# Performance work log

Measured on AMD Instinct MI355X. Metric: run time of the kernel, lower is better.

The kernel has to match this reference:

```python
import jax, jax.numpy as jnp
from jax import lax
import numpy as np

B, M, C, H, W = 32, 2, 256, 16, 16
N = H * W            # 256, square case required by the original bmm chain
DIM = 256            # hardcoded self.dim in the module
THR = 0.1
RATIO = 0.8


def conv2d(x, w, b):
    y = lax.conv_general_dilated(x, w, (1, 1), 'SAME',
                                 dimension_numbers=('NCHW', 'OIHW', 'NCHW'))
    return y + b[None, :, None, None]


def setup_inputs() -> dict:
    key = jax.random.key(0)
    ks = jax.random.split(key, 8)
    return {
        'con_feat': jax.random.normal(ks[0], (B, M, C, H, W), jnp.float32),
        'feat_s':   jax.random.normal(ks[1], (B, M, C, C), jnp.float32),
        'feat_v':   jax.random.uniform(ks[2], (B, M, C), jnp.float32),
        'feat_d':   jax.random.normal(ks[3], (B, M, N, N), jnp.float32),
        'w_enc':    jax.random.normal(ks[4], (C, C, 3, 3), jnp.float32) * 0.02,
        'b_enc':    jnp.zeros((C,), jnp.float32),
        'w_dec':    jax.random.normal(ks[5], (C, C, 3, 3), jnp.float32) * 0.02,
        'b_dec':    jnp.zeros((C,), jnp.float32),
        'w_val':    jax.random.normal(ks[6], (1, 2 * C, 3, 3), jnp.float32) * 0.02,
        'b_val':    jnp.zeros((1,), jnp.float32),
    }


def _assemble(fs, fv, fd, counts):
    # fs: (M,C,C) row blocks, fv: (M,C) diag values, fd: (M,N,N) col blocks, counts: (M,)
    big = max(C, N)                                  # out-of-range sentinel -> dropped
    off = jnp.cumsum(counts) - counts                # exclusive prefix offsets (M,)
    r = jnp.arange(C)
    dest = off[:, None] + r[None, :]                 # (M,C) destination slots
    valid = (r[None, :] < counts[:, None]) & (dest >= 0)
    dest = jnp.where(valid, dest, big).reshape(-1)   # (M*C,)
    ns = jnp.zeros((C, C), fs.dtype).at[dest].set(fs.reshape(M * C, C), mode='drop')
    fd_cols = fd[:, :, :C].transpose(0, 2, 1).reshape(M * C, N)  # source columns as rows
    ndT = jnp.zeros((N, N), fd.dtype).at[dest].set(fd_cols, mode='drop')
    nv = jnp.zeros((C, N), fv.dtype).at[dest, dest].set(fv.reshape(-1), mode='drop')
    return ns, nv, ndT.T


def reference(con_feat, feat_s, feat_v, feat_d, w_enc, b_enc, w_dec, b_dec, w_val, b_val):
    x = con_feat.reshape(B * M, C, H, W)
    # autoencoder reconstruction loss (training branch)
    mid = jax.nn.relu(conv2d(x, w_enc, b_enc))
    x_rec = conv2d(mid, w_dec, b_dec)
    auto_enc_loss = jnp.mean((x - x_rec) ** 2)

    # data-dependent rank budget per (batch, modality)
    counts = jnp.sum(feat_v > THR, axis=-1).astype(jnp.int32)      # (B,M)
    total = jnp.sum(counts, axis=-1)                               # (B,)
    kmin = min(C, N)
    adj = jnp.round(kmin * counts.astype(jnp.float32)
                    / jnp.maximum(total, 1)[:, None].astype(jnp.float32)).astype(jnp.int32)
    if M > 1:
        adj = adj.at[:, -1].set(DIM - jnp.sum(adj[:, :-1], axis=-1))
    counts = jnp.maximum(jnp.where((total > kmin)[:, None], adj, counts), 0)

    # scatter-assemble s/v/d and reconstruct
    ns, nv, nd = jax.vmap(_assemble)(feat_s, feat_v, feat_d, counts)
    rec = jnp.matmul(jnp.matmul(ns, nv), nd)                        # (B,C,N)
    rec = rec.reshape(B, C, H, W)
    rec = conv2d(rec, w_dec, b_dec)                                 # decoder
    rec = (rec - rec.min()) / (rec.max() - rec.min()) * 2.0 - 1.0

    # per-modality value scores, softmax over modality
    scores = jnp.stack([
        jax.nn.sigmoid(jax.nn.relu(conv2d(
            jnp.concatenate([rec, con_feat[:, m]], axis=1), w_val, b_val)))
        for m in range(M)
    ], axis=1)                                                      # (B,M,1,H,W)
    scores = jax.nn.softmax(scores, axis=1)
    fused = jnp.sum((1.0 - RATIO) * scores * con_feat, axis=1) + rec * RATIO
    return fused, auto_enc_loss
```

## Files before the change

kernel.cpp:

```cpp
#include <hip/hip_runtime.h>
#include <math.h>


typedef __attribute__((ext_vector_type(8))) short short8;
typedef __attribute__((ext_vector_type(4))) float f32x4;

__device__ __forceinline__ void gload_lds16(const void* g, void* l) {
  __builtin_amdgcn_global_load_lds(
      (const __attribute__((address_space(1))) void*)g,
      (__attribute__((address_space(3))) void*)l, 16, 0, 0);
}

__device__ __forceinline__ unsigned short f2bf(float f) {
  unsigned u = __float_as_uint(f);
  unsigned r = (u + 0x7FFFu + ((u >> 16) & 1u)) >> 16;
  return (unsigned short)r;
}

__device__ __forceinline__ unsigned mapf(float f) {
  unsigned u = __float_as_uint(f);
  return (u & 0x80000000u) ? ~u : (u | 0x80000000u);
}
__device__ __forceinline__ float unmapf(unsigned u) {
  unsigned v = (u & 0x80000000u) ? (u & 0x7fffffffu) : ~u;
  return __uint_as_float(v);
}

__global__ __launch_bounds__(256) void prep_k(
    const float* __restrict__ cf, const float* __restrict__ we,
    const float* __restrict__ wd, const float* __restrict__ fv,
    unsigned short* __restrict__ Xp, unsigned short* __restrict__ WrE,
    unsigned short* __restrict__ WrD, int* __restrict__ smr,
    float* __restrict__ vd, float4* __restrict__ sraw4,
    float* __restrict__ lacc, unsigned* __restrict__ mm) {
  const int bx = blockIdx.x, t = threadIdx.x;
  if (bx < 2048) {
    int idx = bx * 256 + t;
    int p = idx & 255, ch = (idx >> 8) & 31, img = idx >> 13;
    int ic0 = ch * 8;
    const float* sp = cf + (size_t)img * 65536 + (size_t)ic0 * 256 + p;
    unsigned short h[8];
#pragma unroll
    for (int i = 0; i < 8; ++i) h[i] = f2bf(sp[i * 256]);
    int y = p >> 4, x = p & 15;
    uint4 u;
    u.x = h[0] | (h[1] << 16); u.y = h[2] | (h[3] << 16);
    u.z = h[4] | (h[5] << 16); u.w = h[6] | (h[7] << 16);
    *(uint4*)&Xp[(size_t)img * 82944 + (size_t)(y * 18 + x + 19) * 256 + ic0] = u;
  } else if (bx < 2624) {
    int idx = (bx - 2048) * 256 + t;
    int ch = idx & 31, rest = idx >> 5;
    int s = rest % 9, ocx = rest / 9;
    int oc = ocx & 255, cv = ocx >> 8;
    const float* w = cv ? wd : we;
    unsigned short* o = cv ? WrD : WrE;
    int ic0 = ch * 8;
    unsigned short h[8];
#pragma unroll
    for (int i = 0; i < 8; ++i) h[i] = f2bf(w[(size_t)oc * 2304 + (ic0 + i) * 9 + s]);
    uint4 u;
    u.x = h[0] | (h[1] << 16); u.y = h[2] | (h[3] << 16);
    u.z = h[4] | (h[5] << 16); u.w = h[6] | (h[7] << 16);
    *(uint4*)&o[(size_t)oc * 2304 + s * 256 + ic0] = u;
  } else if (bx < 2752) {
    int img = bx - 2624;
    uint4* base = (uint4*)Xp + (size_t)img * 10368;
    uint4 z; z.x = z.y = z.z = z.w = 0;
    for (int it = t; it < 2176; it += 256) {
      int px = it >> 5, c = it & 31;
      int y, x;
      if (px < 18)      { y = 0;  x = px; }
      else if (px < 36) { y = 17; x = px - 18; }
      else if (px < 52) { y = px - 35; x = 0; }
      else              { y = px - 51; x = 17; }
      base[(y * 18 + x) * 32 + c] = z;
    }
  } else if (bx < 2784) {
    const int b = bx - 2752;
    const float v0 = fv[(size_t)b * 512 + t];
    const float v1 = fv[(size_t)b * 512 + 256 + t];
    const unsigned long long bal0 = __ballot(v0 > 0.1f);
    const unsigned long long bal1 = __ballot(v1 > 0.1f);
    __shared__ int cnt0[4], cnt1[4], fc[2];
    const int wid = t >> 6, lane = t & 63;
    if (lane == 0) { cnt0[wid] = __popcll(bal0); cnt1[wid] = __popcll(bal1); }
    smr[b * 256 + t] = -1;
    vd[b * 256 + t] = 0.f;
    __syncthreads();
    if (t == 0) {
      int c0 = cnt0[0] + cnt0[1] + cnt0[2] + cnt0[3];
      int c1 = cnt1[0] + cnt1[1] + cnt1[2] + cnt1[3];
      int total = c0 + c1;
      int f0, f1;
      if (total > 256) {
        int a0 = (int)rintf(256.0f * (float)c0 / (float)total);
        f0 = a0; f1 = 256 - a0;
      } else { f0 = c0; f1 = c1; }
      fc[0] = max(f0, 0); fc[1] = max(f1, 0);
    }
    __syncthreads();
    const int c0 = fc[0], c1 = fc[1];
    if (t < c0) { smr[b * 256 + t] = t; vd[b * 256 + t] = v0; }
    if (t < c1) {
      int d = c0 + t;
      if (d < 256) { smr[b * 256 + d] = 256 + t; vd[b * 256 + d] = v1; }
    }
  } else {
    int z = bx - 2784;
    if (z < 24) {
      float4 zz; zz.x = zz.y = zz.z = zz.w = 0.f;
      sraw4[z * 256 + t] = zz;
    } else if (t == 0) {
      lacc[0] = 0.f; mm[0] = 0xFFFFFFFFu; mm[1] = 0u;
    }
  }
}

__global__ __launch_bounds__(256) void ansbmt_k(
    const float* __restrict__ fs, const float* __restrict__ fd,
    const int* __restrict__ smr, const float* __restrict__ vd,
    unsigned short* __restrict__ Ans, unsigned short* __restrict__ BmT,
    unsigned short* __restrict__ Recp) {
  const int bx = blockIdx.x, t = threadIdx.x;
  if (bx < 1024) {
    int idx = bx * 256 + t;
    int ch = idx & 31, c = (idx >> 5) & 255, b = idx >> 13;
    int j0 = ch * 8;
    int si = smr[b * 256 + c];
    unsigned short h[8] = {0, 0, 0, 0, 0, 0, 0, 0};
    if (si >= 0) {
      int m = si >> 8, r = si & 255;
      const float* fp = fs + (((size_t)b * 2 + m) * 256 + r) * 256 + j0;
      const float* vp = vd + b * 256 + j0;
#pragma unroll
      for (int i = 0; i < 8; ++i) h[i] = f2bf(fp[i] * vp[i]);
    }
    uint4 u;
    u.x = h[0] | (h[1] << 16); u.y = h[2] | (h[3] << 16);
    u.z = h[4] | (h[5] << 16); u.w = h[6] | (h[7] << 16);
    *(uint4*)&Ans[(size_t)b * 65536 + c * 256 + j0] = u;
  } else if (bx < 1152) {
    __shared__ float sIn[4096];
    const int b = (bx - 1024) >> 2, bz = (bx - 1024) & 3;
    const int sp = smr[b * 256 + t];
    const int m_p = sp >> 8, r_p = sp & 255;
    for (int jg = bz * 8; jg < bz * 8 + 8; ++jg) {
      __syncthreads();
#pragma unroll
      for (int u = 0; u < 4; ++u) {
        int q = t * 4 + u;
        int rr = q >> 6, w = q & 63;
        int m = rr >> 3, i = rr & 7;
        float4 f = ((const float4*)fd)[((size_t)(b * 2 + m) * 256 + jg * 8 + i) * 64 + w];
        *(float4*)&sIn[i * 512 + m * 256 + w * 4] = f;
      }
      __syncthreads();
      unsigned short h[8] = {0, 0, 0, 0, 0, 0, 0, 0};
      if (sp >= 0) {
#pragma unroll
        for (int i = 0; i < 8; ++i) h[i] = f2bf(sIn[i * 512 + m_p * 256 + r_p]);
      }
      uint4 u;
      u.x = h[0] | (h[1] << 16); u.y = h[2] | (h[3] << 16);
      u.z = h[4] | (h[5] << 16); u.w = h[6] | (h[7] << 16);
      *(uint4*)&BmT[(size_t)b * 65536 + t * 256 + jg * 8] = u;
    }
  } else {
    int img = bx - 1152;
    uint4* base = (uint4*)Recp + (size_t)img * 10368;
    uint4 z; z.x = z.y = z.z = z.w = 0;
    for (int it = t; it < 2176; it += 256) {
      int px = it >> 5, c = it & 31;
      int y, x;
      if (px < 18)      { y = 0;  x = px; }
      else if (px < 36) { y = 17; x = px - 18; }
      else if (px < 52) { y = px - 35; x = 0; }
      else              { y = px - 51; x = 17; }
      base[(y * 18 + x) * 32 + c] = z;
    }
  }
}


__global__ __launch_bounds__(512, 4) void encrec_k(
    const unsigned short* __restrict__ Xin, const unsigned short* __restrict__ Wr,
    const float* __restrict__ bias, unsigned short* __restrict__ Midp,
    const unsigned short* __restrict__ BmT, const unsigned short* __restrict__ Ans,
    unsigned short* __restrict__ Recp) {
  __shared__ __align__(16) char S[65536];
  const int t = threadIdx.x, lane = t & 63, wave = t >> 6;
  const int ksplit = wave >> 2, wq = wave & 3;
  const int mw = wq >> 1, nw = wq & 1;
  const int mlane = lane & 15, quad = lane >> 4;
  const int L = blockIdx.x;
  const bool isConv = L < 256;

  int img = 0, b = 0, pt, ot, nkits;
  const char *Ag, *Bg;
  int laneA[2], laneB[2];
  if (isConv) {
    int xcd = L & 7, sl = L >> 3;
    img = xcd * 8 + (sl & 7);
    int tile = sl >> 3;
    pt = tile >> 1; ot = tile & 1;
    Ag = (const char*)Xin + (size_t)img * 165888;
    Bg = (const char*)Wr;
#pragma unroll
    for (int r = 0; r < 2; ++r) {
      int id = r * 512 + t;
      int row = id >> 3, sub = id & 7, q = sub ^ (row & 7);
      int p = pt * 128 + row, y = p >> 4, x = p & 15;
      laneA[r] = (y * 18 + x) * 512 + q * 16;
      laneB[r] = (ot * 128 + row) * 4608 + q * 16;
    }
    nkits = 36;
  } else {
    int l2 = L - 256;
    b = l2 >> 2;
    int tile = l2 & 3;
    pt = tile >> 1; ot = tile & 1;
    Ag = (const char*)BmT + (size_t)b * 131072;
    Bg = (const char*)Ans + (size_t)b * 131072;
#pragma unroll
    for (int r = 0; r < 2; ++r) {
      int id = r * 512 + t;
      int row = id >> 3, sub = id & 7, q = sub ^ (row & 7);
      laneA[r] = (pt * 128 + row) * 512 + q * 16;
      laneB[r] = (ot * 128 + row) * 512 + q * 16;
    }
    nkits = 4;
  }

  int aoff[4], boff[4];
#pragma unroll
  for (int i = 0; i < 4; ++i) {
    int rowm = mw * 64 + i * 16 + mlane;
    aoff[i] = rowm * 128 + (((ksplit * 4 + quad) ^ (rowm & 7)) * 16);
    int rown = nw * 64 + i * 16 + mlane;
    boff[i] = 16384 + rown * 128 + (((ksplit * 4 + quad) ^ (rown & 7)) * 16);
  }

  auto stage = [&](int kit, int buf) {
    int aG, bG = kit * 128;
    if (isConv) {
      int s = kit >> 2;
      int dy = s / 3, dx = s - dy * 3;
      aG = (dy * 18 + dx) * 512 + (kit & 3) * 128;
    } else {
      aG = kit * 128;
    }
    char* dst = S + buf * 32768;
#pragma unroll
    for (int r = 0; r < 2; ++r)
      gload_lds16(Ag + laneA[r] + aG, dst + r * 8192 + wave * 1024);
#pragma unroll
    for (int r = 0; r < 2; ++r)
      gload_lds16(Bg + laneB[r] + bG, dst + 16384 + r * 8192 + wave * 1024);
  };

  f32x4 acc[4][4] = {};
  for (int preload = 0; preload < 1; ++preload) stage(0, 0);
  for (int kit = 0; kit < nkits; ++kit) {
    int cur = kit & 1;
    asm volatile("s_waitcnt vmcnt(0)" ::: "memory");
    asm volatile("s_barrier" ::: "memory");
    if (kit + 1 < nkits) stage(kit + 1, 1 - cur);
    const char* Sb = S + cur * 32768;
    short8 af[4], bf[4];
#pragma unroll
    for (int i = 0; i < 4; ++i) {
      af[i] = *(const short8*)(Sb + aoff[i]);
      bf[i] = *(const short8*)(Sb + boff[i]);
    }
#pragma unroll
    for (int i = 0; i < 4; ++i)
#pragma unroll
      for (int n = 0; n < 4; ++n)
        acc[i][n] = __builtin_amdgcn_mfma_f32_16x16x32_bf16(af[i], bf[n], acc[i][n], 0, 0, 0);
  }

  __syncthreads();
  if (ksplit == 1) {
#pragma unroll
    for (int i = 0; i < 4; ++i)
#pragma unroll
      for (int n = 0; n < 4; ++n)
        *(f32x4*)(S + wq * 16384 + (i * 4 + n) * 1024 + lane * 16) = acc[i][n];
  }
  __syncthreads();
  if (ksplit == 0) {
#pragma unroll
    for (int i = 0; i < 4; ++i)
#pragma unroll
      for (int n = 0; n < 4; ++n)
        acc[i][n] += *(const f32x4*)(S + wq * 16384 + (i * 4 + n) * 1024 + lane * 16);
    if (isConv) {
#pragma unroll
      for (int i = 0; i < 4; ++i) {
        int m0 = pt * 128 + mw * 64 + i * 16 + quad * 4;
#pragma unroll
        for (int n = 0; n < 4; ++n) {
          int oc = ot * 128 + nw * 64 + n * 16 + mlane;
          float bv = bias[oc];
#pragma unroll
          for (int r = 0; r < 4; ++r) {
            int p = m0 + r;
            int y = p >> 4, x = p & 15;
            float v = fmaxf(acc[i][n][r] + bv, 0.f);
            Midp[(size_t)img * 82944 + (size_t)(y * 18 + x + 19) * 256 + oc] = f2bf(v);
          }
        }
      }
    } else {
#pragma unroll
      for (int i = 0; i < 4; ++i) {
        int m0 = pt * 128 + mw * 64 + i * 16 + quad * 4;
#pragma unroll
        for (int n = 0; n < 4; ++n) {
          int cc = ot * 128 + nw * 64 + n * 16 + mlane;
#pragma unroll
          for (int r = 0; r < 4; ++r) {
            int p = m0 + r;
            int y = p >> 4, x = p & 15;
            Recp[(size_t)b * 82944 + (size_t)(y * 18 + x + 19) * 256 + cc] = f2bf(acc[i][n][r]);
          }
        }
      }
    }
  }
}

__global__ __launch_bounds__(512, 4) void conv_dec_k(
    const unsigned short* __restrict__ Midp, const unsigned short* __restrict__ Recp,
    const unsigned short* __restrict__ Wr, const float* __restrict__ bias,
    const float* __restrict__ cfref, float* __restrict__ rec2,
    float* __restrict__ lacc, unsigned* __restrict__ mm) {
  __shared__ __align__(16) char S[65536];
  __shared__ float sred[4], smn[4], smx[4];
  const int t = threadIdx.x, lane = t & 63, wave = t >> 6;
  const int ksplit = wave >> 2, wq = wave & 3;
  const int mw = wq >> 1, nw = wq & 1;
  const int mlane = lane & 15, quad = lane >> 4;
  const int L = blockIdx.x;
  const int xcd = L & 7, sl = L >> 3;
  const int u12 = sl % 12, tile = sl / 12;
  const int unit = xcd * 12 + u12;
  const bool isLoss = unit < 64;
  const int pt = tile >> 1, ot = tile & 1;

  int laneA[2], laneB[2];
#pragma unroll
  for (int r = 0; r < 2; ++r) {
    int id = r * 512 + t;
    int row = id >> 3, sub = id & 7, q = sub ^ (row & 7);
    int p = pt * 128 + row, y = p >> 4, x = p & 15;
    laneA[r] = (y * 18 + x) * 512 + q * 16;
    laneB[r] = (ot * 128 + row) * 4608 + q * 16;
  }
  const char* Ag = isLoss ? (const char*)Midp + (size_t)unit * 165888
                          : (const char*)Recp + (size_t)(unit - 64) * 165888;
  const char* Bg = (const char*)Wr;

  int aoff[4], boff[4];
#pragma unroll
  for (int i = 0; i < 4; ++i) {
    int rowm = mw * 64 + i * 16 + mlane;
    aoff[i] = rowm * 128 + (((ksplit * 4 + quad) ^ (rowm & 7)) * 16);
    int rown = nw * 64 + i * 16 + mlane;
    boff[i] = 16384 + rown * 128 + (((ksplit * 4 + quad) ^ (rown & 7)) * 16);
  }

  auto stage = [&](int kit, int buf) {
    int s = kit >> 2;
    int dy = s / 3, dx = s - dy * 3;
    int aG = (dy * 18 + dx) * 512 + (kit & 3) * 128;
    int bG = kit * 128;
    char* dst = S + buf * 32768;
#pragma unroll
    for (int r = 0; r < 2; ++r)
      gload_lds16(Ag + laneA[r] + aG, dst + r * 8192 + wave * 1024);
#pragma unroll
    for (int r = 0; r < 2; ++r)
      gload_lds16(Bg + laneB[r] + bG, dst + 16384 + r * 8192 + wave * 1024);
  };

  f32x4 acc[4][4] = {};
  stage(0, 0);
  for (int kit = 0; kit < 36; ++kit) {
    int cur = kit & 1;
    asm volatile("s_waitcnt vmcnt(0)" ::: "memory");
    asm volatile("s_barrier" ::: "memory");
    if (kit + 1 < 36) stage(kit + 1, 1 - cur);
    const char* Sb = S + cur * 32768;
    short8 af[4], bf[4];
#pragma unroll
    for (int i = 0; i < 4; ++i) {
      af[i] = *(const short8*)(Sb + aoff[i]);
      bf[i] = *(const short8*)(Sb + boff[i]);
    }
#pragma unroll
    for (int i = 0; i < 4; ++i)
#pragma unroll
      for (int n = 0; n < 4; ++n)
        acc[i][n] = __builtin_amdgcn_mfma_f32_16x16x32_bf16(af[i], bf[n], acc[i][n], 0, 0, 0);
  }

  __syncthreads();
  if (ksplit == 1) {
#pragma unroll
    for (int i = 0; i < 4; ++i)
#pragma unroll
      for (int n = 0; n < 4; ++n)
        *(f32x4*)(S + wq * 16384 + (i * 4 + n) * 1024 + lane * 16) = acc[i][n];
  }
  __syncthreads();
  if (ksplit == 0) {
#pragma unroll
    for (int i = 0; i < 4; ++i)
#pragma unroll
      for (int n = 0; n < 4; ++n)
        acc[i][n] += *(const f32x4*)(S + wq * 16384 + (i * 4 + n) * 1024 + lane * 16);

    if (isLoss) {
      float ls = 0.f;
#pragma unroll
      for (int i = 0; i < 4; ++i) {
        int m0 = pt * 128 + mw * 64 + i * 16 + quad * 4;
#pragma unroll
        for (int n = 0; n < 4; ++n) {
          int oc = ot * 128 + nw * 64 + n * 16 + mlane;
          float bv = bias[oc];
          float4 c4 = *(const float4*)(cfref + (size_t)unit * 65536 + (size_t)oc * 256 + m0);
          float d0 = acc[i][n][0] + bv - c4.x;
          float d1 = acc[i][n][1] + bv - c4.y;
          float d2 = acc[i][n][2] + bv - c4.z;
          float d3 = acc[i][n][3] + bv - c4.w;
          ls += d0 * d0 + d1 * d1 + d2 * d2 + d3 * d3;
        }
      }
#pragma unroll
      for (int off = 32; off; off >>= 1) ls += __shfl_down(ls, off);
      if (lane == 0) sred[wq] = ls;
    } else {
      const int img2 = unit - 64;
      float mn = INFINITY, mx = -INFINITY;
#pragma unroll
      for (int i = 0; i < 4; ++i) {
        int m0 = pt * 128 + mw * 64 + i * 16 + quad * 4;
#pragma unroll
        for (int n = 0; n < 4; ++n) {
          int oc = ot * 128 + nw * 64 + n * 16 + mlane;
          float bv = bias[oc];
          float4 v;
          v.x = acc[i][n][0] + bv; v.y = acc[i][n][1] + bv;
          v.z = acc[i][n][2] + bv; v.w = acc[i][n][3] + bv;
          mn = fminf(mn, fminf(fminf(v.x, v.y), fminf(v.z, v.w)));
          mx = fmaxf(mx, fmaxf(fmaxf(v.x, v.y), fmaxf(v.z, v.w)));
          *(float4*)(rec2 + (size_t)img2 * 65536 + (size_t)oc * 256 + m0) = v;
        }
      }
#pragma unroll
      for (int off = 32; off; off >>= 1) {
        mn = fminf(mn, __shfl_down(mn, off));
        mx = fmaxf(mx, __shfl_down(mx, off));
      }
      if (lane == 0) { smn[wq] = mn; smx[wq] = mx; }
    }
  }
  __syncthreads();
  if (t == 0) {
    if (isLoss) {
      atomicAdd(lacc, sred[0] + sred[1] + sred[2] + sred[3]);
    } else {
      float a = fminf(fminf(smn[0], smn[1]), fminf(smn[2], smn[3]));
      float b2 = fmaxf(fmaxf(smx[0], smx[1]), fmaxf(smx[2], smx[3]));
      atomicMin(&mm[0], mapf(a));
      atomicMax(&mm[1], mapf(b2));
    }
  }
}

__global__ __launch_bounds__(256) void score_conv_k(
    const float* __restrict__ rec2, const float* __restrict__ cf,
    const float* __restrict__ wval, const unsigned* __restrict__ mm,
    float* __restrict__ sraw) {
  const int b = blockIdx.x, phase = blockIdx.y, icc = blockIdx.z;
  const int t = threadIdx.x;
  const int row = t >> 4, col = t & 15;
  __shared__ float s_in[8 * 360];
  __shared__ float s_wv[72];
  for (int i = t; i < 8 * 360; i += 256) s_in[i] = 0.f;
  const float* src;
  float sc = 1.f, sh = 0.f;
  int wofs;
  if (phase == 0) {
    src = rec2 + (size_t)b * 65536;
    float mn = unmapf(mm[0]), mx = unmapf(mm[1]);
    sc = 2.f / (mx - mn);
    sh = -mn * sc - 1.f;
    wofs = 0;
  } else {
    src = cf + ((size_t)b * 2 + (phase - 1)) * 65536;
    wofs = 2304;
  }
  float acc = 0.f;
  for (int ic0 = icc * 32; ic0 < icc * 32 + 32; ic0 += 8) {
    __syncthreads();
#pragma unroll
    for (int i = 0; i < 8; ++i) {
      float v = src[(ic0 + i) * 256 + t];
      if (phase == 0) v = fmaf(v, sc, sh);
      s_in[i * 360 + (row + 1) * 20 + (col + 1)] = v;
    }
    if (t < 72) s_wv[t] = wval[wofs + ic0 * 9 + t];
    __syncthreads();
#pragma unroll
    for (int i = 0; i < 8; ++i)
#pragma unroll
      for (int ky = 0; ky < 3; ++ky)
#pragma unroll
        for (int kx = 0; kx < 3; ++kx)
          acc += s_in[i * 360 + (row + ky) * 20 + (col + kx)] * s_wv[i * 9 + ky * 3 + kx];
  }
  atomicAdd(&sraw[((size_t)b * 3 + phase) * 256 + t], acc);
}

__global__ void fuse_k(const float* __restrict__ cf, const float* __restrict__ rec2,
                       const float* __restrict__ sraw, const float* __restrict__ bval,
                       const unsigned* __restrict__ mm, const float* __restrict__ lacc,
                       float* __restrict__ outp) {
  const int idx = blockIdx.x * 256 + threadIdx.x;
  const int b = idx >> 16;
  const int rest = idx & 65535;
  const int pos = idx & 255;
  const float mn = unmapf(mm[0]), mx = unmapf(mm[1]);
  const float sc = 2.f / (mx - mn), sh = -mn * sc - 1.f;
  const float srec = sraw[(size_t)b * 768 + pos];
  const float sc0 = sraw[(size_t)b * 768 + 256 + pos];
  const float sc1 = sraw[(size_t)b * 768 + 512 + pos];
  const float bv = bval[0];
  const float z0 = fmaxf(srec + sc0 + bv, 0.f);
  const float z1 = fmaxf(srec + sc1 + bv, 0.f);
  const float s0 = 1.f / (1.f + expf(-z0));
  const float s1 = 1.f / (1.f + expf(-z1));
  const float w0 = 1.f / (1.f + expf(s1 - s0));
  const float w1 = 1.f - w0;
  const float rn = fmaf(rec2[idx], sc, sh);
  const float f0 = cf[(size_t)b * 131072 + rest];
  const float f1 = cf[(size_t)b * 131072 + 65536 + rest];
  outp[idx] = 0.2f * (w0 * f0 + w1 * f1) + 0.8f * rn;
  if (idx == 0) outp[2097152] = lacc[0] * (1.f / 4194304.f);
}

extern "C" void kernel_launch(void* const* d_in, const int* in_sizes, int n_in,
                              void* d_out, int out_size, void* d_ws, size_t ws_size,
                              hipStream_t stream) {
  const float* cf    = (const float*)d_in[0];
  const float* fs    = (const float*)d_in[1];
  const float* fv    = (const float*)d_in[2];
  const float* fd    = (const float*)d_in[3];
  const float* w_enc = (const float*)d_in[4];
  const float* b_enc = (const float*)d_in[5];
  const float* w_dec = (const float*)d_in[6];
  const float* b_dec = (const float*)d_in[7];
  const float* w_val = (const float*)d_in[8];
  const float* b_val = (const float*)d_in[9];
  float* out = (float*)d_out;
  float* wsf = (float*)d_ws;

  unsigned short* Xp   = (unsigned short*)wsf;
  unsigned short* Midp = (unsigned short*)(wsf + 2654208);
  unsigned short* Recp = (unsigned short*)(wsf + 5308416);
  float* rec2 = wsf + 6635520;
  unsigned short* WrE = (unsigned short*)(wsf + 8732672);
  unsigned short* WrD = (unsigned short*)(wsf + 9027584);
  unsigned short* Ans = (unsigned short*)(wsf + 9322496);
  unsigned short* BmT = (unsigned short*)(wsf + 10371072);
  float* sraw = wsf + 11419648;
  float* vd   = wsf + 11444224;
  int*   smr  = (int*)(wsf + 11452416);
  float* lacc = wsf + 11460608;
  unsigned* mm = (unsigned*)(wsf + 11460609);

  prep_k<<<2809, 256, 0, stream>>>(cf, w_enc, w_dec, fv, Xp, WrE, WrD, smr, vd,
                                   (float4*)sraw, lacc, mm);
  ansbmt_k<<<1184, 256, 0, stream>>>(fs, fd, smr, vd, Ans, BmT, Recp);
  encrec_k<<<384, 512, 0, stream>>>(Xp, WrE, b_enc, Midp, BmT, Ans, Recp);
  conv_dec_k<<<384, 512, 0, stream>>>(Midp, Recp, WrD, b_dec, cf, rec2, lacc, mm);
  score_conv_k<<<dim3(32, 3, 8), 256, 0, stream>>>(rec2, cf, w_val, mm, sraw);
  fuse_k<<<8192, 256, 0, stream>>>(cf, rec2, sraw, b_val, mm, lacc, out);
}
```

Measured before the change: 217.2 us.

## Fuse prep stages, load GEMM B operand to registers, split score conv

Merges the slot-assignment and Ans/BmT assembly into prep_k by recomputing slot counts per block, which removes one kernel launch and the smr/vd intermediates. The conv and bmm GEMMs now read the B operand straight from global memory into registers, so LDS drops to 32KB and the k-split reduction is staged through it in two halves. The modality score convolutions move into extra encrec_k blocks, letting them overlap with the GEMM. The rec score conv is applied to raw rec2, and the min/max normalisation is folded in afterwards through per-position sums of the weights, which removes the atomics. The costs are redundant ballot work in every prep block and uncoalesced direct global reads of B.

```diff
diff --git a/kernel.cpp b/kernel.cpp
--- a/kernel.cpp
+++ b/kernel.cpp
@@ -26,13 +26,37 @@
   return __uint_as_float(v);
 }
 
+__device__ __forceinline__ void slot_counts(const float* __restrict__ fv, int b,
+                                            int t, int* shm, int& c0o, int& c1o) {
+  const float v0 = fv[(size_t)b * 512 + t];
+  const float v1 = fv[(size_t)b * 512 + 256 + t];
+  const unsigned long long bal0 = __ballot(v0 > 0.1f);
+  const unsigned long long bal1 = __ballot(v1 > 0.1f);
+  const int wid = t >> 6, lane = t & 63;
+  if (lane == 0) { shm[wid] = __popcll(bal0); shm[4 + wid] = __popcll(bal1); }
+  __syncthreads();
+  int c0 = shm[0] + shm[1] + shm[2] + shm[3];
+  int c1 = shm[4] + shm[5] + shm[6] + shm[7];
+  int total = c0 + c1;
+  if (total > 256) {
+    int a0 = (int)rintf(256.0f * (float)c0 / (float)total);
+    c0 = a0; c1 = 256 - a0;
+  }
+  c0o = max(c0, 0); c1o = max(c1, 0);
+}
+
 __global__ __launch_bounds__(256) void prep_k(
     const float* __restrict__ cf, const float* __restrict__ we,
     const float* __restrict__ wd, const float* __restrict__ fv,
+    const float* __restrict__ fs, const float* __restrict__ fd,
+    const float* __restrict__ wval,
     unsigned short* __restrict__ Xp, unsigned short* __restrict__ WrE,
-    unsigned short* __restrict__ WrD, int* __restrict__ smr,
-    float* __restrict__ vd, float4* __restrict__ sraw4,
-    float* __restrict__ lacc, unsigned* __restrict__ mm) {
+    unsigned short* __restrict__ WrD, unsigned short* __restrict__ Ans,
+    unsigned short* __restrict__ BmT, unsigned short* __restrict__ Recp,
+    float* __restrict__ wsum9, float* __restrict__ lacc,
+    unsigned* __restrict__ mm) {
+  __shared__ float sIn[4096];
+  __shared__ int shm[8];
   const int bx = blockIdx.x, t = threadIdx.x;
   if (bx < 2048) {
     int idx = bx * 256 + t;
@@ -76,97 +100,7 @@
       base[(y * 18 + x) * 32 + c] = z;
     }
   } else if (bx < 2784) {
-    const int b = bx - 2752;
-    const float v0 = fv[(size_t)b * 512 + t];
-    const float v1 = fv[(size_t)b * 512 + 256 + t];
-    const unsigned long long bal0 = __ballot(v0 > 0.1f);
-    const unsigned long long bal1 = __ballot(v1 > 0.1f);
-    __shared__ int cnt0[4], cnt1[4], fc[2];
-    const int wid = t >> 6, lane = t & 63;
-    if (lane == 0) { cnt0[wid] = __popcll(bal0); cnt1[wid] = __popcll(bal1); }
-    smr[b * 256 + t] = -1;
-    vd[b * 256 + t] = 0.f;
-    __syncthreads();
-    if (t == 0) {
-      int c0 = cnt0[0] + cnt0[1] + cnt0[2] + cnt0[3];
-      int c1 = cnt1[0] + cnt1[1] + cnt1[2] + cnt1[3];
-      int total = c0 + c1;
-      int f0, f1;
-      if (total > 256) {
-        int a0 = (int)rintf(256.0f * (float)c0 / (float)total);
-        f0 = a0; f1 = 256 - a0;
-      } else { f0 = c0; f1 = c1; }
-      fc[0] = max(f0, 0); fc[1] = max(f1, 0);
-    }
-    __syncthreads();
-    const int c0 = fc[0], c1 = fc[1];
-    if (t < c0) { smr[b * 256 + t] = t; vd[b * 256 + t] = v0; }
-    if (t < c1) {
-      int d = c0 + t;
-      if (d < 256) { smr[b * 256 + d] = 256 + t; vd[b * 256 + d] = v1; }
-    }
-  } else {
-    int z = bx - 2784;
-    if (z < 24) {
-      float4 zz; zz.x = zz.y = zz.z = zz.w = 0.f;
-      sraw4[z * 256 + t] = zz;
-    } else if (t == 0) {
-      lacc[0] = 0.f; mm[0] = 0xFFFFFFFFu; mm[1] = 0u;
-    }
-  }
-}
-
-__global__ __launch_bounds__(256) void ansbmt_k(
-    const float* __restrict__ fs, const float* __restrict__ fd,
-    const int* __restrict__ smr, const float* __restrict__ vd,
-    unsigned short* __restrict__ Ans, unsigned short* __restrict__ BmT,
-    unsigned short* __restrict__ Recp) {
-  const int bx = blockIdx.x, t = threadIdx.x;
-  if (bx < 1024) {
-    int idx = bx * 256 + t;
-    int ch = idx & 31, c = (idx >> 5) & 255, b = idx >> 13;
-    int j0 = ch * 8;
-    int si = smr[b * 256 + c];
-    unsigned short h[8] = {0, 0, 0, 0, 0, 0, 0, 0};
-    if (si >= 0) {
-      int m = si >> 8, r = si & 255;
-      const float* fp = fs + (((size_t)b * 2 + m) * 256 + r) * 256 + j0;
-      const float* vp = vd + b * 256 + j0;
-#pragma unroll
-      for (int i = 0; i < 8; ++i) h[i] = f2bf(fp[i] * vp[i]);
-    }
-    uint4 u;
-    u.x = h[0] | (h[1] << 16); u.y = h[2] | (h[3] << 16);
-    u.z = h[4] | (h[5] << 16); u.w = h[6] | (h[7] << 16);
-    *(uint4*)&Ans[(size_t)b * 65536 + c * 256 + j0] = u;
-  } else if (bx < 1152) {
-    __shared__ float sIn[4096];
-    const int b = (bx - 1024) >> 2, bz = (bx - 1024) & 3;
-    const int sp = smr[b * 256 + t];
-    const int m_p = sp >> 8, r_p = sp & 255;
-    for (int jg = bz * 8; jg < bz * 8 + 8; ++jg) {
-      __syncthreads();
-#pragma unroll
-      for (int u = 0; u < 4; ++u) {
-        int q = t * 4 + u;
-        int rr = q >> 6, w = q & 63;
-        int m = rr >> 3, i = rr & 7;
-        float4 f = ((const float4*)fd)[((size_t)(b * 2 + m) * 256 + jg * 8 + i) * 64 + w];
-        *(float4*)&sIn[i * 512 + m * 256 + w * 4] = f;
-      }
-      __syncthreads();
-      unsigned short h[8] = {0, 0, 0, 0, 0, 0, 0, 0};
-      if (sp >= 0) {
-#pragma unroll
-        for (int i = 0; i < 8; ++i) h[i] = f2bf(sIn[i * 512 + m_p * 256 + r_p]);
-      }
-      uint4 u;
-      u.x = h[0] | (h[1] << 16); u.y = h[2] | (h[3] << 16);
-      u.z = h[4] | (h[5] << 16); u.w = h[6] | (h[7] << 16);
-      *(uint4*)&BmT[(size_t)b * 65536 + t * 256 + jg * 8] = u;
-    }
-  } else {
-    int img = bx - 1152;
+    int img = bx - 2752;
     uint4* base = (uint4*)Recp + (size_t)img * 10368;
     uint4 z; z.x = z.y = z.z = z.w = 0;
     for (int it = t; it < 2176; it += 256) {
@@ -178,26 +112,126 @@
       else              { y = px - 51; x = 17; }
       base[(y * 18 + x) * 32 + c] = z;
     }
-  }
-}
-
+  } else if (bx < 3808) {
+    int bi = bx - 2784;
+    int b = bi >> 5, cbase = (bi & 31) * 8;
+    int c0, c1;
+    slot_counts(fv, b, t, shm, c0, c1);
+    int c = cbase + (t >> 5), ch = t & 31, j0 = ch * 8;
+    int m = -1, r = 0;
+    if (c < c0) { m = 0; r = c; }
+    else if (c - c0 < c1) { m = 1; r = c - c0; }
+    unsigned short h[8] = {0, 0, 0, 0, 0, 0, 0, 0};
+    if (m >= 0) {
+      const float* fp = fs + (((size_t)b * 2 + m) * 256 + r) * 256 + j0;
+#pragma unroll
+      for (int i = 0; i < 8; ++i) {
+        int j = j0 + i;
+        float vj = 0.f;
+        if (j < c0) vj = fv[(size_t)b * 512 + j];
+        else if (j - c0 < c1) vj = fv[(size_t)b * 512 + 256 + (j - c0)];
+        h[i] = f2bf(fp[i] * vj);
+      }
+    }
+    uint4 u;
+    u.x = h[0] | (h[1] << 16); u.y = h[2] | (h[3] << 16);
+    u.z = h[4] | (h[5] << 16); u.w = h[6] | (h[7] << 16);
+    *(uint4*)&Ans[(size_t)b * 65536 + c * 256 + j0] = u;
+  } else if (bx < 3936) {
+    int bi = bx - 3808;
+    int b = bi >> 2, bz = bi & 3;
+    int c0, c1;
+    slot_counts(fv, b, t, shm, c0, c1);
+    int m_p = -1, r_p = 0;
+    if (t < c0) { m_p = 0; r_p = t; }
+    else if (t - c0 < c1) { m_p = 1; r_p = t - c0; }
+    for (int jg = bz * 8; jg < bz * 8 + 8; ++jg) {
+      __syncthreads();
+#pragma unroll
+      for (int u = 0; u < 4; ++u) {
+        int q = t * 4 + u;
+        int rr = q >> 6, w = q & 63;
+        int m = rr >> 3, i = rr & 7;
+        float4 f = ((const float4*)fd)[((size_t)(b * 2 + m) * 256 + jg * 8 + i) * 64 + w];
+        *(float4*)&sIn[i * 512 + m * 256 + w * 4] = f;
+      }
+      __syncthreads();
+      unsigned short h[8] = {0, 0, 0, 0, 0, 0, 0, 0};
+      if (m_p >= 0) {
+#pragma unroll
+        for (int i = 0; i < 8; ++i) h[i] = f2bf(sIn[i * 512 + m_p * 256 + r_p]);
+      }
+      uint4 u;
+      u.x = h[0] | (h[1] << 16); u.y = h[2] | (h[3] << 16);
+      u.z = h[4] | (h[5] << 16); u.w = h[6] | (h[7] << 16);
+      *(uint4*)&BmT[(size_t)b * 65536 + t * 256 + jg * 8] = u;
+    }
+  } else {
+    for (int j = 0; j < 9; ++j) {
+      float v = wval[t * 9 + j];
+#pragma unroll
+      for (int off = 32; off; off >>= 1) v += __shfl_down(v, off);
+      if ((t & 63) == 0) sIn[t >> 6] = v;
+      __syncthreads();
+      if (t == 0) wsum9[j] = sIn[0] + sIn[1] + sIn[2] + sIn[3];
+      __syncthreads();
+    }
+    if (t == 0) { lacc[0] = 0.f; mm[0] = 0xFFFFFFFFu; mm[1] = 0u; }
+  }
+}
 
 __global__ __launch_bounds__(512, 4) void encrec_k(
     const unsigned short* __restrict__ Xin, const unsigned short* __restrict__ Wr,
     const float* __restrict__ bias, unsigned short* __restrict__ Midp,
     const unsigned short* __restrict__ BmT, const unsigned short* __restrict__ Ans,
-    unsigned short* __restrict__ Recp) {
-  __shared__ __align__(16) char S[65536];
+    unsigned short* __restrict__ Recp, const float* __restrict__ cf,
+    const float* __restrict__ wval, float* __restrict__ sraw) {
+  __shared__ __align__(16) char S[32768];
   const int t = threadIdx.x, lane = t & 63, wave = t >> 6;
+  const int L = blockIdx.x;
+
+  if (L >= 384) {
+    const int sb = L - 384;
+    const int b = sb >> 1, m = sb & 1;
+    const int half = t >> 8, px = t & 255;
+    const int row = px >> 4, col = px & 15;
+    float* sf = (float*)S;
+    float* myin = sf + half * 2880;
+    float* mywv = sf + 5760 + half * 72;
+    const float* src = cf + ((size_t)b * 2 + m) * 65536;
+    for (int i = t; i < 5760; i += 512) sf[i] = 0.f;
+    float acc = 0.f;
+    for (int it = 0; it < 16; ++it) {
+      int ic0 = half * 128 + it * 8;
+      __syncthreads();
+#pragma unroll
+      for (int i = 0; i < 8; ++i)
+        myin[i * 360 + (row + 1) * 20 + (col + 1)] = src[(ic0 + i) * 256 + px];
+      if (px < 72) mywv[px] = wval[2304 + ic0 * 9 + px];
+      __syncthreads();
+#pragma unroll
+      for (int i = 0; i < 8; ++i)
+#pragma unroll
+        for (int ky = 0; ky < 3; ++ky)
+#pragma unroll
+          for (int kx = 0; kx < 3; ++kx)
+            acc += myin[i * 360 + (row + ky) * 20 + (col + kx)] * mywv[i * 9 + ky * 3 + kx];
+    }
+    __syncthreads();
+    if (half == 1) sf[5904 + px] = acc;
+    __syncthreads();
+    if (half == 0) sraw[(size_t)b * 768 + (1 + m) * 256 + px] = acc + sf[5904 + px];
+    return;
+  }
+
   const int ksplit = wave >> 2, wq = wave & 3;
   const int mw = wq >> 1, nw = wq & 1;
   const int mlane = lane & 15, quad = lane >> 4;
-  const int L = blockIdx.x;
   const bool isConv = L < 256;
 
   int img = 0, b = 0, pt, ot, nkits;
   const char *Ag, *Bg;
-  int laneA[2], laneB[2];
+  size_t brs;
   if (isConv) {
     int xcd = L & 7, sl = L >> 3;
     img = xcd * 8 + (sl & 7);
@@ -205,15 +239,7 @@
     pt = tile >> 1; ot = tile & 1;
     Ag = (const char*)Xin + (size_t)img * 165888;
     Bg = (const char*)Wr;
-#pragma unroll
-    for (int r = 0; r < 2; ++r) {
-      int id = r * 512 + t;
-      int row = id >> 3, sub = id & 7, q = sub ^ (row & 7);
-      int p = pt * 128 + row, y = p >> 4, x = p & 15;
-      laneA[r] = (y * 18 + x) * 512 + q * 16;
-      laneB[r] = (ot * 128 + row) * 4608 + q * 16;
-    }
-    nkits = 36;
+    brs = 4608; nkits = 36;
   } else {
     int l2 = L - 256;
     b = l2 >> 2;
@@ -221,27 +247,36 @@
     pt = tile >> 1; ot = tile & 1;
     Ag = (const char*)BmT + (size_t)b * 131072;
     Bg = (const char*)Ans + (size_t)b * 131072;
-#pragma unroll
-    for (int r = 0; r < 2; ++r) {
-      int id = r * 512 + t;
-      int row = id >> 3, sub = id & 7, q = sub ^ (row & 7);
+    brs = 512; nkits = 4;
+  }
+
+  int laneA[2];
+#pragma unroll
+  for (int r = 0; r < 2; ++r) {
+    int id = r * 512 + t;
+    int row = id >> 3, sub = id & 7, q = sub ^ (row & 7);
+    if (isConv) {
+      int p = pt * 128 + row, y = p >> 4, x = p & 15;
+      laneA[r] = (y * 18 + x) * 512 + q * 16;
+    } else {
       laneA[r] = (pt * 128 + row) * 512 + q * 16;
-      laneB[r] = (ot * 128 + row) * 512 + q * 16;
-    }
-    nkits = 4;
-  }
-
-  int aoff[4], boff[4];
+    }
+  }
+  int aoff[4];
 #pragma unroll
   for (int i = 0; i < 4; ++i) {
     int rowm = mw * 64 + i * 16 + mlane;
     aoff[i] = rowm * 128 + (((ksplit * 4 + quad) ^ (rowm & 7)) * 16);
-    int rown = nw * 64 + i * 16 + mlane;
-    boff[i] = 16384 + rown * 128 + (((ksplit * 4 + quad) ^ (rown & 7)) * 16);
-  }
-
-  auto stage = [&](int kit, int buf) {
-    int aG, bG = kit * 128;
+  }
+  const char* pB[4];
+#pragma unroll
+  for (int n = 0; n < 4; ++n) {
+    int rowb = ot * 128 + nw * 64 + n * 16 + mlane;
+    pB[n] = Bg + (size_t)rowb * brs + ksplit * 64 + quad * 16;
+  }
+
+  auto stageA = [&](int kit, int buf) {
+    int aG;
     if (isConv) {
       int s = kit >> 2;
       int dy = s / 3, dx = s - dy * 3;
@@ -249,81 +284,78 @@
     } else {
       aG = kit * 128;
     }
-    char* dst = S + buf * 32768;
+    char* dst = S + buf * 16384;
 #pragma unroll
     for (int r = 0; r < 2; ++r)
       gload_lds16(Ag + laneA[r] + aG, dst + r * 8192 + wave * 1024);
-#pragma unroll
-    for (int r = 0; r < 2; ++r)
-      gload_lds16(Bg + laneB[r] + bG, dst + 16384 + r * 8192 + wave * 1024);
   };
 
   f32x4 acc[4][4] = {};
-  for (int preload = 0; preload < 1; ++preload) stage(0, 0);
-  for (int kit = 0; kit < nkits; ++kit) {
-    int cur = kit & 1;
+  short8 bf0[4], bf1[4];
+  auto loadB = [&](int kit, short8* bf) {
+#pragma unroll
+    for (int n = 0; n < 4; ++n) bf[n] = *(const short8*)(pB[n] + kit * 128);
+  };
+  auto compute = [&](int buf, short8* bf) {
+    const char* Sb = S + buf * 16384;
+#pragma unroll
+    for (int i = 0; i < 4; ++i) {
+      short8 af = *(const short8*)(Sb + aoff[i]);
+#pragma unroll
+      for (int n = 0; n < 4; ++n)
+        acc[i][n] = __builtin_amdgcn_mfma_f32_16x16x32_bf16(af, bf[n], acc[i][n], 0, 0, 0);
+    }
+  };
+
+  stageA(0, 0); loadB(0, bf0);
+  for (int kit = 0; kit < nkits; kit += 2) {
     asm volatile("s_waitcnt vmcnt(0)" ::: "memory");
     asm volatile("s_barrier" ::: "memory");
-    if (kit + 1 < nkits) stage(kit + 1, 1 - cur);
-    const char* Sb = S + cur * 32768;
-    short8 af[4], bf[4];
+    if (kit + 1 < nkits) { stageA(kit + 1, 1); loadB(kit + 1, bf1); }
+    compute(0, bf0);
+    asm volatile("s_waitcnt vmcnt(0)" ::: "memory");
+    asm volatile("s_barrier" ::: "memory");
+    if (kit + 2 < nkits) { stageA(kit + 2, 0); loadB(kit + 2, bf0); }
+    compute(1, bf1);
+  }
+
+  __syncthreads();
+#pragma unroll
+  for (int rr = 0; rr < 2; ++rr) {
+    if (ksplit == 1 && (wq >> 1) == rr) {
+#pragma unroll
+      for (int i = 0; i < 4; ++i)
+#pragma unroll
+        for (int n = 0; n < 4; ++n)
+          *(f32x4*)(S + (wq & 1) * 16384 + (i * 4 + n) * 1024 + lane * 16) = acc[i][n];
+    }
+    __syncthreads();
+    if (ksplit == 0 && (wq >> 1) == rr) {
+#pragma unroll
+      for (int i = 0; i < 4; ++i)
+#pragma unroll
+        for (int n = 0; n < 4; ++n)
+          acc[i][n] += *(const f32x4*)(S + (wq & 1) * 16384 + (i * 4 + n) * 1024 + lane * 16);
+    }
+    __syncthreads();
+  }
+
+  if (ksplit == 0) {
+    unsigned short* ob = isConv ? Midp + (size_t)img * 82944 : Recp + (size_t)b * 82944;
 #pragma unroll
     for (int i = 0; i < 4; ++i) {
-      af[i] = *(const short8*)(Sb + aoff[i]);
-      bf[i] = *(const short8*)(Sb + boff[i]);
-    }
-#pragma unroll
-    for (int i = 0; i < 4; ++i)
-#pragma unroll
-      for (int n = 0; n < 4; ++n)
-        acc[i][n] = __builtin_amdgcn_mfma_f32_16x16x32_bf16(af[i], bf[n], acc[i][n], 0, 0, 0);
-  }
-
-  __syncthreads();
-  if (ksplit == 1) {
-#pragma unroll
-    for (int i = 0; i < 4; ++i)
-#pragma unroll
-      for (int n = 0; n < 4; ++n)
-        *(f32x4*)(S + wq * 16384 + (i * 4 + n) * 1024 + lane * 16) = acc[i][n];
-  }
-  __syncthreads();
-  if (ksplit == 0) {
-#pragma unroll
-    for (int i = 0; i < 4; ++i)
-#pragma unroll
-      for (int n = 0; n < 4; ++n)
-        acc[i][n] += *(const f32x4*)(S + wq * 16384 + (i * 4 + n) * 1024 + lane * 16);
-    if (isConv) {
-#pragma unroll
-      for (int i = 0; i < 4; ++i) {
-        int m0 = pt * 128 + mw * 64 + i * 16 + quad * 4;
-#pragma unroll
-        for (int n = 0; n < 4; ++n) {
-          int oc = ot * 128 + nw * 64 + n * 16 + mlane;
-          float bv = bias[oc];
-#pragma unroll
-          for (int r = 0; r < 4; ++r) {
-            int p = m0 + r;
-            int y = p >> 4, x = p & 15;
-            float v = fmaxf(acc[i][n][r] + bv, 0.f);
-            Midp[(size_t)img * 82944 + (size_t)(y * 18 + x + 19) * 256 + oc] = f2bf(v);
-          }
-        }
-      }
-    } else {
-#pragma unroll
-      for (int i = 0; i < 4; ++i) {
-        int m0 = pt * 128 + mw * 64 + i * 16 + quad * 4;
-#pragma unroll
-        for (int n = 0; n < 4; ++n) {
-          int cc = ot * 128 + nw * 64 + n * 16 + mlane;
-#pragma unroll
-          for (int r = 0; r < 4; ++r) {
-            int p = m0 + r;
-            int y = p >> 4, x = p & 15;
-            Recp[(size_t)b * 82944 + (size_t)(y * 18 + x + 19) * 256 + cc] = f2bf(acc[i][n][r]);
-          }
+      int m0 = pt * 128 + mw * 64 + i * 16 + quad * 4;
+#pragma unroll
+      for (int n = 0; n < 4; ++n) {
+        int oc = ot * 128 + nw * 64 + n * 16 + mlane;
+        float bv = isConv ? bias[oc] : 0.f;
+#pragma unroll
+        for (int r = 0; r < 4; ++r) {
+          int p = m0 + r;
+          int y = p >> 4, x = p & 15;
+          float v = acc[i][n][r] + bv;
+          if (isConv) v = fmaxf(v, 0.f);
+          ob[(size_t)(y * 18 + x + 19) * 256 + oc] = f2bf(v);
         }
       }
     }
@@ -335,7 +367,7 @@
     const unsigned short* __restrict__ Wr, const float* __restrict__ bias,
     const float* __restrict__ cfref, float* __restrict__ rec2,
     float* __restrict__ lacc, unsigned* __restrict__ mm) {
-  __shared__ __align__(16) char S[65536];
+  __shared__ __align__(16) char S[32768];
   __shared__ float sred[4], smn[4], smx[4];
   const int t = threadIdx.x, lane = t & 63, wave = t >> 6;
   const int ksplit = wave >> 2, wq = wave & 3;
@@ -348,79 +380,92 @@
   const bool isLoss = unit < 64;
   const int pt = tile >> 1, ot = tile & 1;
 
-  int laneA[2], laneB[2];
+  int laneA[2];
 #pragma unroll
   for (int r = 0; r < 2; ++r) {
     int id = r * 512 + t;
     int row = id >> 3, sub = id & 7, q = sub ^ (row & 7);
     int p = pt * 128 + row, y = p >> 4, x = p & 15;
     laneA[r] = (y * 18 + x) * 512 + q * 16;
-    laneB[r] = (ot * 128 + row) * 4608 + q * 16;
   }
   const char* Ag = isLoss ? (const char*)Midp + (size_t)unit * 165888
                           : (const char*)Recp + (size_t)(unit - 64) * 165888;
   const char* Bg = (const char*)Wr;
 
-  int aoff[4], boff[4];
+  int aoff[4];
 #pragma unroll
   for (int i = 0; i < 4; ++i) {
     int rowm = mw * 64 + i * 16 + mlane;
     aoff[i] = rowm * 128 + (((ksplit * 4 + quad) ^ (rowm & 7)) * 16);
-    int rown = nw * 64 + i * 16 + mlane;
-    boff[i] = 16384 + rown * 128 + (((ksplit * 4 + quad) ^ (rown & 7)) * 16);
-  }
-
-  auto stage = [&](int kit, int buf) {
+  }
+  const char* pB[4];
+#pragma unroll
+  for (int n = 0; n < 4; ++n) {
+    int rowb = ot * 128 + nw * 64 + n * 16 + mlane;
+    pB[n] = Bg + (size_t)rowb * 4608 + ksplit * 64 + quad * 16;
+  }
+
+  auto stageA = [&](int kit, int buf) {
     int s = kit >> 2;
     int dy = s / 3, dx = s - dy * 3;
     int aG = (dy * 18 + dx) * 512 + (kit & 3) * 128;
-    int bG = kit * 128;
-    char* dst = S + buf * 32768;
+    char* dst = S + buf * 16384;
 #pragma unroll
     for (int r = 0; r < 2; ++r)
       gload_lds16(Ag + laneA[r] + aG, dst + r * 8192 + wave * 1024);
-#pragma unroll
-    for (int r = 0; r < 2; ++r)
-      gload_lds16(Bg + laneB[r] + bG, dst + 16384 + r * 8192 + wave * 1024);
   };
 
   f32x4 acc[4][4] = {};
-  stage(0, 0);
-  for (int kit = 0; kit < 36; ++kit) {
-    int cur = kit & 1;
+  short8 bf0[4], bf1[4];
+  auto loadB = [&](int kit, short8* bf) {
+#pragma unroll
+    for (int n = 0; n < 4; ++n) bf[n] = *(const short8*)(pB[n] + kit * 128);
+  };
+  auto compute = [&](int buf, short8* bf) {
+    const char* Sb = S + buf * 16384;
+#pragma unroll
+    for (int i = 0; i < 4; ++i) {
+      short8 af = *(const short8*)(Sb + aoff[i]);
+#pragma unroll
+      for (int n = 0; n < 4; ++n)
+        acc[i][n] = __builtin_amdgcn_mfma_f32_16x16x32_bf16(af, bf[n], acc[i][n], 0, 0, 0);
+    }
+  };
+
+  stageA(0, 0); loadB(0, bf0);
+  for (int kit = 0; kit < 36; kit += 2) {
     asm volatile("s_waitcnt vmcnt(0)" ::: "memory");
     asm volatile("s_barrier" ::: "memory");
-    if (kit + 1 < 36) stage(kit + 1, 1 - cur);
-    const char* Sb = S + cur * 32768;
-    short8 af[4], bf[4];
-#pragma unroll
-    for (int i = 0; i < 4; ++i) {
-      af[i] = *(const short8*)(Sb + aoff[i]);
-      bf[i] = *(const short8*)(Sb + boff[i]);
-    }
-#pragma unroll
-    for (int i = 0; i < 4; ++i)
-#pragma unroll
-      for (int n = 0; n < 4; ++n)
-        acc[i][n] = __builtin_amdgcn_mfma_f32_16x16x32_bf16(af[i], bf[n], acc[i][n], 0, 0, 0);
+    if (kit + 1 < 36) { stageA(kit + 1, 1); loadB(kit + 1, bf1); }
+    compute(0, bf0);
+    asm volatile("s_waitcnt vmcnt(0)" ::: "memory");
+    asm volatile("s_barrier" ::: "memory");
+    if (kit + 2 < 36) { stageA(kit + 2, 0); loadB(kit + 2, bf0); }
+    compute(1, bf1);
   }
 
   __syncthreads();
-  if (ksplit == 1) {
-#pragma unroll
-    for (int i = 0; i < 4; ++i)
-#pragma unroll
-      for (int n = 0; n < 4; ++n)
-        *(f32x4*)(S + wq * 16384 + (i * 4 + n) * 1024 + lane * 16) = acc[i][n];
-  }
-  __syncthreads();
+#pragma unroll
+  for (int rr = 0; rr < 2; ++rr) {
+    if (ksplit == 1 && (wq >> 1) == rr) {
+#pragma unroll
+      for (int i = 0; i < 4; ++i)
+#pragma unroll
+        for (int n = 0; n < 4; ++n)
+          *(f32x4*)(S + (wq & 1) * 16384 + (i * 4 + n) * 1024 + lane * 16) = acc[i][n];
+    }
+    __syncthreads();
+    if (ksplit == 0 && (wq >> 1) == rr) {
+#pragma unroll
+      for (int i = 0; i < 4; ++i)
+#pragma unroll
+        for (int n = 0; n < 4; ++n)
+          acc[i][n] += *(const f32x4*)(S + (wq & 1) * 16384 + (i * 4 + n) * 1024 + lane * 16);
+    }
+    __syncthreads();
+  }
+
   if (ksplit == 0) {
-#pragma unroll
-    for (int i = 0; i < 4; ++i)
-#pragma unroll
-      for (int n = 0; n < 4; ++n)
-        acc[i][n] += *(const f32x4*)(S + wq * 16384 + (i * 4 + n) * 1024 + lane * 16);
-
     if (isLoss) {
       float ls = 0.f;
 #pragma unroll
@@ -480,62 +525,64 @@
   }
 }
 
-__global__ __launch_bounds__(256) void score_conv_k(
-    const float* __restrict__ rec2, const float* __restrict__ cf,
-    const float* __restrict__ wval, const unsigned* __restrict__ mm,
+__global__ __launch_bounds__(512) void score_rec_k(
+    const float* __restrict__ rec2, const float* __restrict__ wval,
     float* __restrict__ sraw) {
-  const int b = blockIdx.x, phase = blockIdx.y, icc = blockIdx.z;
-  const int t = threadIdx.x;
-  const int row = t >> 4, col = t & 15;
-  __shared__ float s_in[8 * 360];
-  __shared__ float s_wv[72];
-  for (int i = t; i < 8 * 360; i += 256) s_in[i] = 0.f;
-  const float* src;
-  float sc = 1.f, sh = 0.f;
-  int wofs;
-  if (phase == 0) {
-    src = rec2 + (size_t)b * 65536;
-    float mn = unmapf(mm[0]), mx = unmapf(mm[1]);
-    sc = 2.f / (mx - mn);
-    sh = -mn * sc - 1.f;
-    wofs = 0;
-  } else {
-    src = cf + ((size_t)b * 2 + (phase - 1)) * 65536;
-    wofs = 2304;
-  }
+  __shared__ float sf[6160];
+  const int b = blockIdx.x, t = threadIdx.x;
+  const int half = t >> 8, px = t & 255;
+  const int row = px >> 4, col = px & 15;
+  float* myin = sf + half * 2880;
+  float* mywv = sf + 5760 + half * 72;
+  const float* src = rec2 + (size_t)b * 65536;
+  for (int i = t; i < 5760; i += 512) sf[i] = 0.f;
   float acc = 0.f;
-  for (int ic0 = icc * 32; ic0 < icc * 32 + 32; ic0 += 8) {
-    __syncthreads();
-#pragma unroll
-    for (int i = 0; i < 8; ++i) {
-      float v = src[(ic0 + i) * 256 + t];
-      if (phase == 0) v = fmaf(v, sc, sh);
-      s_in[i * 360 + (row + 1) * 20 + (col + 1)] = v;
-    }
-    if (t < 72) s_wv[t] = wval[wofs + ic0 * 9 + t];
+  for (int it = 0; it < 16; ++it) {
+    int ic0 = half * 128 + it * 8;
     __syncthreads();
 #pragma unroll
     for (int i = 0; i < 8; ++i)
+      myin[i * 360 + (row + 1) * 20 + (col + 1)] = src[(ic0 + i) * 256 + px];
+    if (px < 72) mywv[px] = wval[ic0 * 9 + px];
+    __syncthreads();
+#pragma unroll
+    for (int i = 0; i < 8; ++i)
 #pragma unroll
       for (int ky = 0; ky < 3; ++ky)
 #pragma unroll
         for (int kx = 0; kx < 3; ++kx)
-          acc += s_in[i * 360 + (row + ky) * 20 + (col + kx)] * s_wv[i * 9 + ky * 3 + kx];
-  }
-  atomicAdd(&sraw[((size_t)b * 3 + phase) * 256 + t], acc);
+          acc += myin[i * 360 + (row + ky) * 20 + (col + kx)] * mywv[i * 9 + ky * 3 + kx];
+  }
+  __syncthreads();
+  if (half == 1) sf[5904 + px] = acc;
+  __syncthreads();
+  if (half == 0) sraw[(size_t)b * 768 + px] = acc + sf[5904 + px];
 }
 
 __global__ void fuse_k(const float* __restrict__ cf, const float* __restrict__ rec2,
                        const float* __restrict__ sraw, const float* __restrict__ bval,
                        const unsigned* __restrict__ mm, const float* __restrict__ lacc,
-                       float* __restrict__ outp) {
+                       const float* __restrict__ wsum9, float* __restrict__ outp) {
   const int idx = blockIdx.x * 256 + threadIdx.x;
   const int b = idx >> 16;
   const int rest = idx & 65535;
   const int pos = idx & 255;
   const float mn = unmapf(mm[0]), mx = unmapf(mm[1]);
   const float sc = 2.f / (mx - mn), sh = -mn * sc - 1.f;
-  const float srec = sraw[(size_t)b * 768 + pos];
+  const int y = pos >> 4, x = pos & 15;
+  float P = 0.f;
+#pragma unroll
+  for (int ky = 0; ky < 3; ++ky) {
+    int yy = y + ky - 1;
+    if (yy < 0 || yy > 15) continue;
+#pragma unroll
+    for (int kx = 0; kx < 3; ++kx) {
+      int xx = x + kx - 1;
+      if (xx < 0 || xx > 15) continue;
+      P += wsum9[ky * 3 + kx];
+    }
+  }
+  const float srec = sc * sraw[(size_t)b * 768 + pos] + sh * P;
   const float sc0 = sraw[(size_t)b * 768 + 256 + pos];
   const float sc1 = sraw[(size_t)b * 768 + 512 + pos];
   const float bv = bval[0];
@@ -577,16 +624,15 @@
   unsigned short* Ans = (unsigned short*)(wsf + 9322496);
   unsigned short* BmT = (unsigned short*)(wsf + 10371072);
   float* sraw = wsf + 11419648;
-  float* vd   = wsf + 11444224;
-  int*   smr  = (int*)(wsf + 11452416);
-  float* lacc = wsf + 11460608;
-  unsigned* mm = (unsigned*)(wsf + 11460609);
-
-  prep_k<<<2809, 256, 0, stream>>>(cf, w_enc, w_dec, fv, Xp, WrE, WrD, smr, vd,
-                                   (float4*)sraw, lacc, mm);
-  ansbmt_k<<<1184, 256, 0, stream>>>(fs, fd, smr, vd, Ans, BmT, Recp);
-  encrec_k<<<384, 512, 0, stream>>>(Xp, WrE, b_enc, Midp, BmT, Ans, Recp);
+  float* wsum9 = wsf + 11444224;
+  float* lacc = wsf + 11444240;
+  unsigned* mm = (unsigned*)(wsf + 11444241);
+
+  prep_k<<<3937, 256, 0, stream>>>(cf, w_enc, w_dec, fv, fs, fd, w_val,
+                                   Xp, WrE, WrD, Ans, BmT, Recp, wsum9, lacc, mm);
+  encrec_k<<<448, 512, 0, stream>>>(Xp, WrE, b_enc, Midp, BmT, Ans, Recp,
+                                    cf, w_val, sraw);
   conv_dec_k<<<384, 512, 0, stream>>>(Midp, Recp, WrD, b_dec, cf, rec2, lacc, mm);
-  score_conv_k<<<dim3(32, 3, 8), 256, 0, stream>>>(rec2, cf, w_val, mm, sraw);
-  fuse_k<<<8192, 256, 0, stream>>>(cf, rec2, sraw, b_val, mm, lacc, out);
-}
+  score_rec_k<<<32, 512, 0, stream>>>(rec2, w_val, sraw);
+  fuse_k<<<8192, 256, 0, stream>>>(cf, rec2, sraw, b_val, mm, lacc, wsum9, out);
+}
```

Result: slower. 312.6 us (+43.9%).
